# Performance work log

Hardware: AMD Instinct MI355X
Metric: run time of the kernel (lower is better)

The kernel has to match this reference:

```python
import jax, jax.numpy as jnp
import numpy as np
from jax import lax

B, T, F = 2048, 512, 8
C = 16   # conv out channels
H = 10   # lstm hidden size


def setup_inputs() -> dict:
    key = jax.random.key(0)
    ks = jax.random.split(key, 12)
    s_conv = 1.0 / np.sqrt(F * 3)
    s1 = 1.0 / np.sqrt(H)
    inp = {
        'x': jax.random.normal(ks[0], (B, T, F), dtype=jnp.float32),
        'conv_w': jax.random.uniform(ks[1], (C, F, 3), jnp.float32, -s_conv, s_conv),
        'conv_b': jax.random.uniform(ks[2], (C,), jnp.float32, -s_conv, s_conv),
        'w_ih1': jax.random.uniform(ks[3], (4 * H, C), jnp.float32, -s1, s1),
        'w_hh1': jax.random.uniform(ks[4], (4 * H, H), jnp.float32, -s1, s1),
        'b_ih1': jax.random.uniform(ks[5], (4 * H,), jnp.float32, -s1, s1),
        'b_hh1': jax.random.uniform(ks[6], (4 * H,), jnp.float32, -s1, s1),
        'w_ih2': jax.random.uniform(ks[7], (4 * H, H), jnp.float32, -s1, s1),
        'w_hh2': jax.random.uniform(ks[8], (4 * H, H), jnp.float32, -s1, s1),
        'b_ih2': jax.random.uniform(ks[9], (4 * H,), jnp.float32, -s1, s1),
        'b_hh2': jax.random.uniform(ks[9], (4 * H,), jnp.float32, -s1, s1),
        'lin_w': jax.random.uniform(ks[10], (1, H), jnp.float32, -s1, s1),
        'lin_b': jax.random.uniform(ks[11], (1,), jnp.float32, -s1, s1),
    }
    return inp


def _lstm(seq, w_ih, w_hh, b_ih, b_hh):
    # seq: [B, T, D] -> hidden stream [B, T, H]; PyTorch gate order i,f,g,o.
    xg = jnp.einsum('btd,gd->btg', seq, w_ih) + (b_ih + b_hh)  # [B,T,4H]
    h0 = jnp.zeros((seq.shape[0], H), seq.dtype)

    def step(carry, xg_t):
        h, c = carry
        g = xg_t + h @ w_hh.T
        i, f, gg, o = jnp.split(g, 4, axis=-1)
        c = jax.nn.sigmoid(f) * c + jax.nn.sigmoid(i) * jnp.tanh(gg)
        h = jax.nn.sigmoid(o) * jnp.tanh(c)
        return (h, c), h

    _, hs = lax.scan(step, (h0, h0), jnp.swapaxes(xg, 0, 1))  # [T,B,H]
    return jnp.swapaxes(hs, 0, 1)


def reference(x, conv_w, conv_b, w_ih1, w_hh1, b_ih1, b_hh1,
              w_ih2, w_hh2, b_ih2, b_hh2, lin_w, lin_b):
    # conv1d over time, padding=1 keeps length (dropout is identity in eval)
    xc = jnp.transpose(x, (0, 2, 1))  # [B,F,T]
    y = lax.conv_general_dilated(xc, conv_w, window_strides=(1,),
                                 padding=[(1, 1)],
                                 dimension_numbers=('NCH', 'OIH', 'NCH'))
    y = jax.nn.relu(y + conv_b[None, :, None])
    y = jnp.transpose(y, (0, 2, 1))  # [B,T,C]
    h1 = _lstm(y, w_ih1, w_hh1, b_ih1, b_hh1)
    h2 = _lstm(h1, w_ih2, w_hh2, b_ih2, b_hh2)
    last = h2[:, -1, :]  # [B,H]
    return jax.nn.sigmoid(last @ lin_w.T + lin_b)  # [B,1]
```

## Files before the change

### kernel.cpp

```cpp
#include <hip/hip_runtime.h>

#define TT 512
#define FF 8
#define CC 16
#define HH 10

__device__ __forceinline__ float rl(float v, int k){
    return __int_as_float(__builtin_amdgcn_readlane(__float_as_int(v), k));
}
__device__ __forceinline__ float sigf(float z){
    return __builtin_amdgcn_rcpf(1.f + __expf(-z));
}
__device__ __forceinline__ float tanh_f(float z){
    return 1.f - 2.f * __builtin_amdgcn_rcpf(1.f + __expf(2.f * z));
}

#define CONV_Y(Y) do{                                                                              \
    float a0 = cb, a1 = 0.f;                                                                       \
    a0 = fmaf(w0a.x, cw[0],  a0); a1 = fmaf(w1a.x, cw[1],  a1); a0 = fmaf(w2a.x, cw[2],  a0);      \
    a1 = fmaf(w0a.y, cw[3],  a1); a0 = fmaf(w1a.y, cw[4],  a0); a1 = fmaf(w2a.y, cw[5],  a1);      \
    a0 = fmaf(w0a.z, cw[6],  a0); a1 = fmaf(w1a.z, cw[7],  a1); a0 = fmaf(w2a.z, cw[8],  a0);      \
    a1 = fmaf(w0a.w, cw[9],  a1); a0 = fmaf(w1a.w, cw[10], a0); a1 = fmaf(w2a.w, cw[11], a1);      \
    a0 = fmaf(w0b.x, cw[12], a0); a1 = fmaf(w1b.x, cw[13], a1); a0 = fmaf(w2b.x, cw[14], a0);      \
    a1 = fmaf(w0b.y, cw[15], a1); a0 = fmaf(w1b.y, cw[16], a0); a1 = fmaf(w2b.y, cw[17], a1);      \
    a0 = fmaf(w0b.z, cw[18], a0); a1 = fmaf(w1b.z, cw[19], a1); a0 = fmaf(w2b.z, cw[20], a0);      \
    a1 = fmaf(w0b.w, cw[21], a1); a0 = fmaf(w1b.w, cw[22], a0); a1 = fmaf(w2b.w, cw[23], a1);      \
    Y = fmaxf(a0 + a1, 0.f);                                                                       \
}while(0)

#define H1BCAST                                                                                    \
    const float hs0=rl(h1,0), hs1=rl(h1,1), hs2=rl(h1,2), hs3=rl(h1,3), hs4=rl(h1,4),              \
                hs5=rl(h1,5), hs6=rl(h1,6), hs7=rl(h1,7), hs8=rl(h1,8), hs9=rl(h1,9);

#define LAYER2 do{                                                                                 \
    float d0 = b2, d1 = 0.f;                                                                       \
    d0 = fmaf(hs0, wih2[0], d0);  d1 = fmaf(hs1, wih2[1], d1);                                     \
    d0 = fmaf(hs2, wih2[2], d0);  d1 = fmaf(hs3, wih2[3], d1);                                     \
    d0 = fmaf(hs4, wih2[4], d0);  d1 = fmaf(hs5, wih2[5], d1);                                     \
    d0 = fmaf(hs6, wih2[6], d0);  d1 = fmaf(hs7, wih2[7], d1);                                     \
    d0 = fmaf(hs8, wih2[8], d0);  d1 = fmaf(hs9, wih2[9], d1);                                     \
    d0 = fmaf(rl(h2,0), whh2[0], d0);  d1 = fmaf(rl(h2,1), whh2[1], d1);                           \
    d0 = fmaf(rl(h2,2), whh2[2], d0);  d1 = fmaf(rl(h2,3), whh2[3], d1);                           \
    d0 = fmaf(rl(h2,4), whh2[4], d0);  d1 = fmaf(rl(h2,5), whh2[5], d1);                           \
    d0 = fmaf(rl(h2,6), whh2[6], d0);  d1 = fmaf(rl(h2,7), whh2[7], d1);                           \
    d0 = fmaf(rl(h2,8), whh2[8], d0);  d1 = fmaf(rl(h2,9), whh2[9], d1);                           \
    const float g2  = d0 + d1;                                                                     \
    const float z2  = isG ? (g2 + g2) : g2;                                                        \
    const float sg2 = sigf(z2);                                                                    \
    const float act2 = isG ? fmaf(2.f, sg2, -1.f) : sg2;                                           \
    const float ai2 = __shfl(act2, u,      64);                                                    \
    const float af2 = __shfl(act2, u + 10, 64);                                                    \
    const float ag2 = __shfl(act2, u + 20, 64);                                                    \
    const float ao2 = __shfl(act2, u + 30, 64);                                                    \
    c2 = fmaf(af2, c2, ai2 * ag2);                                                                 \
    h2 = ao2 * tanh_f(c2);                                                                         \
}while(0)

#define LAYER1(YV) do{                                                                             \
    float s0 = b1, s1 = 0.f;                                                                       \
    s0 = fmaf(rl(YV,0),  wih1[0],  s0);  s1 = fmaf(rl(YV,1),  wih1[1],  s1);                       \
    s0 = fmaf(rl(YV,2),  wih1[2],  s0);  s1 = fmaf(rl(YV,3),  wih1[3],  s1);                       \
    s0 = fmaf(rl(YV,4),  wih1[4],  s0);  s1 = fmaf(rl(YV,5),  wih1[5],  s1);                       \
    s0 = fmaf(rl(YV,6),  wih1[6],  s0);  s1 = fmaf(rl(YV,7),  wih1[7],  s1);                       \
    s0 = fmaf(rl(YV,8),  wih1[8],  s0);  s1 = fmaf(rl(YV,9),  wih1[9],  s1);                       \
    s0 = fmaf(rl(YV,10), wih1[10], s0);  s1 = fmaf(rl(YV,11), wih1[11], s1);                       \
    s0 = fmaf(rl(YV,12), wih1[12], s0);  s1 = fmaf(rl(YV,13), wih1[13], s1);                       \
    s0 = fmaf(rl(YV,14), wih1[14], s0);  s1 = fmaf(rl(YV,15), wih1[15], s1);                       \
    s0 = fmaf(hs0, whh1[0], s0);  s1 = fmaf(hs1, whh1[1], s1);                                     \
    s0 = fmaf(hs2, whh1[2], s0);  s1 = fmaf(hs3, whh1[3], s1);                                     \
    s0 = fmaf(hs4, whh1[4], s0);  s1 = fmaf(hs5, whh1[5], s1);                                     \
    s0 = fmaf(hs6, whh1[6], s0);  s1 = fmaf(hs7, whh1[7], s1);                                     \
    s0 = fmaf(hs8, whh1[8], s0);  s1 = fmaf(hs9, whh1[9], s1);                                     \
    const float g1  = s0 + s1;                                                                     \
    const float z1  = isG ? (g1 + g1) : g1;                                                        \
    const float sg1 = sigf(z1);                                                                    \
    const float act1 = isG ? fmaf(2.f, sg1, -1.f) : sg1;                                           \
    const float ai1 = __shfl(act1, u,      64);                                                    \
    const float af1 = __shfl(act1, u + 10, 64);                                                    \
    const float ag1 = __shfl(act1, u + 20, 64);                                                    \
    const float ao1 = __shfl(act1, u + 30, 64);                                                    \
    c1 = fmaf(af1, c1, ai1 * ag1);                                                                 \
    h1n = ao1 * tanh_f(c1);                                                                        \
}while(0)

__global__ __launch_bounds__(64, 2)
void lstm_fused(const float* __restrict__ x,
                const float* __restrict__ conv_w, const float* __restrict__ conv_b,
                const float* __restrict__ w_ih1,  const float* __restrict__ w_hh1,
                const float* __restrict__ b_ih1,  const float* __restrict__ b_hh1,
                const float* __restrict__ w_ih2,  const float* __restrict__ w_hh2,
                const float* __restrict__ b_ih2,  const float* __restrict__ b_hh2,
                const float* __restrict__ lin_w,  const float* __restrict__ lin_b,
                float* __restrict__ out)
{
    const int lane  = threadIdx.x;
    const int batch = blockIdx.x;
    const int grow  = (lane < 40) ? lane : 39;
    const int q     = grow / 10;
    const int u     = grow - q * 10;
    const int ch    = lane & 15;
    const bool isG  = (q == 2);

    float cw[24];
    #pragma unroll
    for (int m = 0; m < 24; ++m) cw[m] = conv_w[ch*24 + m];
    const float cb = conv_b[ch];

    float wih1[CC], whh1[HH], wih2[HH], whh2[HH];
    #pragma unroll
    for (int k = 0; k < CC; ++k) wih1[k] = w_ih1[grow*CC + k];
    #pragma unroll
    for (int k = 0; k < HH; ++k){
        whh1[k] = w_hh1[grow*HH + k];
        wih2[k] = w_ih2[grow*HH + k];
        whh2[k] = w_hh2[grow*HH + k];
    }
    const float b1 = b_ih1[grow] + b_hh1[grow];
    const float b2 = b_ih2[grow] + b_hh2[grow];

    const float* xb = x + (size_t)batch * (TT*FF);

    float h1 = 0.f, c1 = 0.f, h2 = 0.f, c2 = 0.f, h1n;

    float4 w0a = make_float4(0.f,0.f,0.f,0.f), w0b = w0a;
    float4 w1a = *(const float4*)(xb + 0);
    float4 w1b = *(const float4*)(xb + 4);
    float4 w2a = *(const float4*)(xb + 8);
    float4 w2b = *(const float4*)(xb + 12);

    {
        float y0; CONV_Y(y0);
        H1BCAST;
        LAYER1(y0);
        h1 = h1n;
    }
    w0a = w1a; w0b = w1b; w1a = w2a; w1b = w2b;
    w2a = *(const float4*)(xb + 16);
    w2b = *(const float4*)(xb + 20);

    #pragma unroll 3
    for (int t = 1; t < TT; ++t){
        float4 nxa = make_float4(0.f,0.f,0.f,0.f), nxb = nxa;
        if (t + 2 < TT){
            const float* p = xb + (t+2)*FF;
            nxa = *(const float4*)p;
            nxb = *(const float4*)(p + 4);
        }
        float y; CONV_Y(y);
        {
            H1BCAST;
            LAYER2;
            LAYER1(y);
        }
        h1 = h1n;
        w0a = w1a; w0b = w1b; w1a = w2a; w1b = w2b; w2a = nxa; w2b = nxb;
    }

    {
        H1BCAST;
        LAYER2;
    }

    float part = (lane < HH) ? h2 * lin_w[lane] : 0.f;
    #pragma unroll
    for (int off = 8; off > 0; off >>= 1) part += __shfl_xor(part, off, 16);
    if (lane == 0) out[batch] = sigf(part + lin_b[0]);
}

extern "C" void kernel_launch(void* const* d_in, const int* in_sizes, int n_in,
                              void* d_out, int out_size, void* d_ws, size_t ws_size,
                              hipStream_t stream) {
    const float* x      = (const float*)d_in[0];
    const float* conv_w = (const float*)d_in[1];
    const float* conv_b = (const float*)d_in[2];
    const float* w_ih1  = (const float*)d_in[3];
    const float* w_hh1  = (const float*)d_in[4];
    const float* b_ih1  = (const float*)d_in[5];
    const float* b_hh1  = (const float*)d_in[6];
    const float* w_ih2  = (const float*)d_in[7];
    const float* w_hh2  = (const float*)d_in[8];
    const float* b_ih2  = (const float*)d_in[9];
    const float* b_hh2  = (const float*)d_in[10];
    const float* lin_w  = (const float*)d_in[11];
    const float* lin_b  = (const float*)d_in[12];
    float* out = (float*)d_out;

    lstm_fused<<<dim3(2048), dim3(64), 0, stream>>>(
        x, conv_w, conv_b, w_ih1, w_hh1, b_ih1, b_hh1,
        w_ih2, w_hh2, b_ih2, b_hh2, lin_w, lin_b, out);
}
```

Before: 282.1 us.

## Split conv and layer-1 input projection into parallel precompute kernel before recurrence

Adds a precompute kernel that, per batch, computes the conv1d+ReLU and the layer-1 input gate projection for all timesteps in parallel using shared memory, and writes xg to the workspace. The sequential LSTM kernel then only loads one precomputed value per lane per step, removing the conv and input-projection FMAs from the serial critical path. In exchange it writes and reads about 168 MB of intermediate data through global memory and adds a second launch. It falls back to the fused kernel when the workspace is too small.

New measurement: 346.4 us. +22.8%, slower.

```diff
diff --git a/kernel.cpp b/kernel.cpp
--- a/kernel.cpp
+++ b/kernel.cpp
@@ -4,6 +4,7 @@
 #define FF 8
 #define CC 16
 #define HH 10
+#define G4 40
 
 __device__ __forceinline__ float rl(float v, int k){
     return __int_as_float(__builtin_amdgcn_readlane(__float_as_int(v), k));
@@ -95,7 +96,7 @@
 {
     const int lane  = threadIdx.x;
     const int batch = blockIdx.x;
-    const int grow  = (lane < 40) ? lane : 39;
+    const int grow  = (lane < G4) ? lane : (G4-1);
     const int q     = grow / 10;
     const int u     = grow - q * 10;
     const int ch    = lane & 15;
@@ -155,11 +156,182 @@
         h1 = h1n;
         w0a = w1a; w0b = w1b; w1a = w2a; w1b = w2b; w2a = nxa; w2b = nxb;
     }
-
     {
         H1BCAST;
         LAYER2;
     }
+
+    float part = (lane < HH) ? h2 * lin_w[lane] : 0.f;
+    #pragma unroll
+    for (int off = 8; off > 0; off >>= 1) part += __shfl_xor(part, off, 16);
+    if (lane == 0) out[batch] = sigf(part + lin_b[0]);
+}
+
+__global__ __launch_bounds__(256)
+void precompute_xg(const float* __restrict__ x,
+                   const float* __restrict__ conv_w, const float* __restrict__ conv_b,
+                   const float* __restrict__ w_ih1,  const float* __restrict__ b_ih1,
+                   const float* __restrict__ b_hh1,
+                   float* __restrict__ xg)
+{
+    __shared__ __align__(16) float xs[TT][FF];
+    __shared__ __align__(16) float ys[TT][CC];
+    __shared__ float wl[G4][CC + 1];
+    __shared__ float bl[G4];
+
+    const int tid = threadIdx.x;
+    const int b   = blockIdx.x;
+    const float* xb = x + (size_t)b * (TT*FF);
+
+    for (int i = tid; i < TT*FF/4; i += 256)
+        ((float4*)xs)[i] = ((const float4*)xb)[i];
+    for (int i = tid; i < G4*CC; i += 256){
+        int g = i >> 4, k = i & 15;
+        wl[g][k] = w_ih1[g*CC + k];
+    }
+    if (tid < G4) bl[tid] = b_ih1[tid] + b_hh1[tid];
+    __syncthreads();
+
+    {
+        const int ch  = tid & 15;
+        const int seg = tid >> 4;
+        float cw[24];
+        #pragma unroll
+        for (int m = 0; m < 24; ++m) cw[m] = conv_w[ch*24 + m];
+        const float cb = conv_b[ch];
+        const int t0 = seg * 32;
+        float4 w0a, w0b, w1a, w1b, w2a, w2b;
+        if (t0 == 0){ w0a = make_float4(0.f,0.f,0.f,0.f); w0b = w0a; }
+        else        { w0a = *(const float4*)&xs[t0-1][0]; w0b = *(const float4*)&xs[t0-1][4]; }
+        w1a = *(const float4*)&xs[t0][0]; w1b = *(const float4*)&xs[t0][4];
+        #pragma unroll 4
+        for (int i = 0; i < 32; ++i){
+            const int t = t0 + i;
+            if (t + 1 < TT){ w2a = *(const float4*)&xs[t+1][0]; w2b = *(const float4*)&xs[t+1][4]; }
+            else           { w2a = make_float4(0.f,0.f,0.f,0.f); w2b = w2a; }
+            float y; CONV_Y(y);
+            ys[t][ch] = y;
+            w0a = w1a; w0b = w1b; w1a = w2a; w1b = w2b;
+        }
+    }
+    __syncthreads();
+
+    {
+        int t = tid / G4;
+        int g = tid - t * G4;
+        float* xgb = xg + (size_t)b * (TT*G4);
+        #pragma unroll 4
+        for (int i = 0; i < 80; ++i){
+            const float4 y0 = *(const float4*)&ys[t][0];
+            const float4 y1 = *(const float4*)&ys[t][4];
+            const float4 y2 = *(const float4*)&ys[t][8];
+            const float4 y3 = *(const float4*)&ys[t][12];
+            float s0 = bl[g], s1 = 0.f;
+            s0 = fmaf(y0.x, wl[g][0],  s0);  s1 = fmaf(y0.y, wl[g][1],  s1);
+            s0 = fmaf(y0.z, wl[g][2],  s0);  s1 = fmaf(y0.w, wl[g][3],  s1);
+            s0 = fmaf(y1.x, wl[g][4],  s0);  s1 = fmaf(y1.y, wl[g][5],  s1);
+            s0 = fmaf(y1.z, wl[g][6],  s0);  s1 = fmaf(y1.w, wl[g][7],  s1);
+            s0 = fmaf(y2.x, wl[g][8],  s0);  s1 = fmaf(y2.y, wl[g][9],  s1);
+            s0 = fmaf(y2.z, wl[g][10], s0);  s1 = fmaf(y2.w, wl[g][11], s1);
+            s0 = fmaf(y3.x, wl[g][12], s0);  s1 = fmaf(y3.y, wl[g][13], s1);
+            s0 = fmaf(y3.z, wl[g][14], s0);  s1 = fmaf(y3.w, wl[g][15], s1);
+            xgb[t*G4 + g] = s0 + s1;
+            t += 6; g += 16; if (g >= G4){ g -= G4; ++t; }
+        }
+    }
+}
+
+#define LAYER2B do{                                                               \
+    float d0 = b2, d1 = 0.f;                                                      \
+    d0 = fmaf(hs0, wih2[0], d0);  d1 = fmaf(hs1, wih2[1], d1);                    \
+    d0 = fmaf(hs2, wih2[2], d0);  d1 = fmaf(hs3, wih2[3], d1);                    \
+    d0 = fmaf(hs4, wih2[4], d0);  d1 = fmaf(hs5, wih2[5], d1);                    \
+    d0 = fmaf(hs6, wih2[6], d0);  d1 = fmaf(hs7, wih2[7], d1);                    \
+    d0 = fmaf(hs8, wih2[8], d0);  d1 = fmaf(hs9, wih2[9], d1);                    \
+    d0 = fmaf(rl(h2,0), whh2[0], d0);  d1 = fmaf(rl(h2,1), whh2[1], d1);          \
+    d0 = fmaf(rl(h2,2), whh2[2], d0);  d1 = fmaf(rl(h2,3), whh2[3], d1);          \
+    d0 = fmaf(rl(h2,4), whh2[4], d0);  d1 = fmaf(rl(h2,5), whh2[5], d1);          \
+    d0 = fmaf(rl(h2,6), whh2[6], d0);  d1 = fmaf(rl(h2,7), whh2[7], d1);          \
+    d0 = fmaf(rl(h2,8), whh2[8], d0);  d1 = fmaf(rl(h2,9), whh2[9], d1);          \
+    const float g2  = d0 + d1;                                                    \
+    const float sg2 = sigf(g2 * zM);                                              \
+    const float act2 = fmaf(aA, sg2, aB);                                         \
+    const float ai2 = __shfl(act2, u,      64);                                   \
+    const float af2 = __shfl(act2, u + 10, 64);                                   \
+    const float ag2 = __shfl(act2, u + 20, 64);                                   \
+    const float ao2 = __shfl(act2, u + 30, 64);                                   \
+    c2 = fmaf(af2, c2, ai2 * ag2);                                                \
+    h2 = ao2 * tanh_f(c2);                                                        \
+}while(0)
+
+#define LAYER1B(XGV) do{                                                          \
+    float s0 = (XGV), s1 = 0.f;                                                   \
+    s0 = fmaf(hs0, whh1[0], s0);  s1 = fmaf(hs1, whh1[1], s1);                    \
+    s0 = fmaf(hs2, whh1[2], s0);  s1 = fmaf(hs3, whh1[3], s1);                    \
+    s0 = fmaf(hs4, whh1[4], s0);  s1 = fmaf(hs5, whh1[5], s1);                    \
+    s0 = fmaf(hs6, whh1[6], s0);  s1 = fmaf(hs7, whh1[7], s1);                    \
+    s0 = fmaf(hs8, whh1[8], s0);  s1 = fmaf(hs9, whh1[9], s1);                    \
+    const float g1  = s0 + s1;                                                    \
+    const float sg1 = sigf(g1 * zM);                                              \
+    const float act1 = fmaf(aA, sg1, aB);                                         \
+    const float ai1 = __shfl(act1, u,      64);                                   \
+    const float af1 = __shfl(act1, u + 10, 64);                                   \
+    const float ag1 = __shfl(act1, u + 20, 64);                                   \
+    const float ao1 = __shfl(act1, u + 30, 64);                                   \
+    c1 = fmaf(af1, c1, ai1 * ag1);                                                \
+    h1n = ao1 * tanh_f(c1);                                                       \
+}while(0)
+
+__global__ __launch_bounds__(64, 2)
+void lstm_seq(const float* __restrict__ xg,
+              const float* __restrict__ w_hh1,
+              const float* __restrict__ w_ih2,  const float* __restrict__ w_hh2,
+              const float* __restrict__ b_ih2,  const float* __restrict__ b_hh2,
+              const float* __restrict__ lin_w,  const float* __restrict__ lin_b,
+              float* __restrict__ out)
+{
+    const int lane  = threadIdx.x;
+    const int batch = blockIdx.x;
+    const int grow  = (lane < G4) ? lane : (G4-1);
+    const int q     = grow / 10;
+    const int u     = grow - q * 10;
+    const bool isG  = (q == 2);
+    const float zM = isG ? 2.f : 1.f;
+    const float aA = isG ? 2.f : 1.f;
+    const float aB = isG ? -1.f : 0.f;
+
+    float whh1[HH], wih2[HH], whh2[HH];
+    #pragma unroll
+    for (int k = 0; k < HH; ++k){
+        whh1[k] = w_hh1[grow*HH + k];
+        wih2[k] = w_ih2[grow*HH + k];
+        whh2[k] = w_hh2[grow*HH + k];
+    }
+    const float b2 = b_ih2[grow] + b_hh2[grow];
+
+    const float* xp = xg + (size_t)batch * (TT*G4) + grow;
+
+    float h1 = 0.f, c1 = 0.f, h2 = 0.f, c2 = 0.f, h1n;
+
+    float xgv = xp[0];
+    {
+        H1BCAST;
+        LAYER1B(xgv);
+        h1 = h1n;
+    }
+    float xgnext = xp[G4];
+
+    #pragma unroll 2
+    for (int t = 1; t < TT; ++t){
+        const float xgcur = xgnext;
+        const int tn = (t + 1 < TT) ? (t + 1) : (TT - 1);
+        xgnext = xp[(size_t)tn * G4];
+        H1BCAST;
+        LAYER2B;
+        LAYER1B(xgcur);
+        h1 = h1n;
+    }
+    { H1BCAST; LAYER2B; }
 
     float part = (lane < HH) ? h2 * lin_w[lane] : 0.f;
     #pragma unroll
@@ -185,7 +357,18 @@
     const float* lin_b  = (const float*)d_in[12];
     float* out = (float*)d_out;
 
-    lstm_fused<<<dim3(2048), dim3(64), 0, stream>>>(
-        x, conv_w, conv_b, w_ih1, w_hh1, b_ih1, b_hh1,
-        w_ih2, w_hh2, b_ih2, b_hh2, lin_w, lin_b, out);
-}
+    const int NB = 2048;
+    const size_t XG_BYTES = (size_t)NB * TT * G4 * sizeof(float);
+
+    if (ws_size >= XG_BYTES){
+        float* xgws = (float*)d_ws;
+        precompute_xg<<<dim3(NB), dim3(256), 0, stream>>>(
+            x, conv_w, conv_b, w_ih1, b_ih1, b_hh1, xgws);
+        lstm_seq<<<dim3(NB), dim3(64), 0, stream>>>(
+            xgws, w_hh1, w_ih2, w_hh2, b_ih2, b_hh2, lin_w, lin_b, out);
+    } else {
+        lstm_fused<<<dim3(NB), dim3(64), 0, stream>>>(
+            x, conv_w, conv_b, w_ih1, w_hh1, b_ih1, b_hh1,
+            w_ih2, w_hh2, b_ih2, b_hh2, lin_w, lin_b, out);
+    }
+}
```
